# Performance work log

Measured on AMD Instinct MI355X. Metric: run time of the kernel, lower is better.

## Reference

```python
import jax, jax.numpy as jnp
import numpy as np
from jax import lax

GAP_PENALTY = 0.0
TEMPERATURE = 1.0
B, A, L, D, K = 64, 26, 384, 512, 18


def setup_inputs() -> dict:
    key = jax.random.key(0)
    k1, k2, k3, k4 = jax.random.split(key, 4)
    matrices = jax.random.normal(k1, (B, A, L), dtype=jnp.float32)
    # ragged lengths: (len_i, len_0) per pair, in [L//2, L]
    shapes = jax.random.randint(k2, (B, 2), L // 2, L + 1, dtype=jnp.int32)
    s = 1.0 / np.sqrt(A * K)  # torch Conv1d default init scale
    conv_w = jax.random.uniform(k3, (D, A, K), minval=-s, maxval=s, dtype=jnp.float32)
    conv_b = jax.random.uniform(k4, (D,), minval=-s, maxval=s, dtype=jnp.float32)
    return {"matrices": matrices, "shapes": shapes, "conv_w": conv_w, "conv_b": conv_b}


def _smoothmax3(a, b, c, t):
    # t * log(exp(a/t) + exp(b/t) + exp(c/t)), numerically stable
    m = jnp.maximum(jnp.maximum(a, b), c)
    return m + t * jnp.log(jnp.exp((a - m) / t) + jnp.exp((b - m) / t) + jnp.exp((c - m) / t))


def _nw_matrix(sim, t, g):
    # sim: (L, L). Returns smoothed NW value matrix V: (L+1, L+1).
    # V[i,j] = sim[i-1,j-1] + smoothmax(V[i-1,j-1], V[i-1,j]-g, V[i,j-1]-g)
    n = sim.shape[0]
    row0 = -g * jnp.arange(n + 1, dtype=sim.dtype)  # free/affine leading gaps on top row

    def row_step(prev_row, inp):
        s_row, i = inp  # s_row: (L,)
        v_left0 = -g * i  # V[i, 0]

        def col_step(left, xs):
            s, diag, up = xs
            v = s + _smoothmax3(diag, up - g, left - g, t)
            return v, v

        _, rest = lax.scan(col_step, v_left0, (s_row, prev_row[:-1], prev_row[1:]))
        new_row = jnp.concatenate([v_left0[None], rest])
        return new_row, new_row

    _, rows = lax.scan(row_step, row0, (sim, jnp.arange(1, n + 1, dtype=sim.dtype)))
    return jnp.concatenate([row0[None], rows], axis=0)


def needleman_wunsch(sim, shapes, gap_penalty, temperature):
    # sim: (B, L, L) similarity vs sequence 0; shapes: (B, 2) int lengths.
    # Soft alignment posterior = grad of smoothed terminal score wrt similarity.
    li = jnp.clip(shapes[:, 0], 0, sim.shape[1])
    lj = jnp.clip(shapes[:, 1], 0, sim.shape[2])

    def total_score(s):
        V = jax.vmap(lambda m: _nw_matrix(m, temperature, gap_penalty))(s)  # (B, L+1, L+1)
        b = jnp.arange(s.shape[0])
        return jnp.sum(V[b, li, lj])

    return jax.grad(total_score)(sim)  # (B, L, L), expected match matrix


def reference(matrices, shapes, conv_w, conv_b):
    # Conv1d padding='same' with even kernel: torch pads (k-1)//2 left, k//2 right
    k = conv_w.shape[-1]
    pad = ((k - 1) // 2, k // 2)
    emb = lax.conv_general_dilated(
        matrices, conv_w, window_strides=(1,), padding=[pad],
        dimension_numbers=("NCH", "OIH", "NCH"),
    ) + conv_b[None, :, None]  # (B, D, L)
    e = jnp.transpose(emb, (0, 2, 1))  # (B, L, D)
    sim = jnp.einsum("bld,md->blm", e, e[0])  # (B, L_i, L_0): similarity vs sequence 0
    align = needleman_wunsch(sim, shapes, GAP_PENALTY, TEMPERATURE)  # (B, L, L)
    m = jnp.transpose(matrices, (0, 2, 1))  # (B, L, A)
    # consensus in sequence-0 coordinates, then project back to each sequence
    consensus = jnp.mean(jnp.einsum("nia,nij->nja", m, align), axis=0)  # (L, A)
    return jnp.einsum("ja,nij->nia", consensus, align)  # (B, L, A)
```

## Files before the change

### kernel.cpp

```cpp
#include <hip/hip_runtime.h>
#include <hip/hip_bf16.h>
#include <math.h>

#define B_  64
#define A_  26
#define L_  384
#define D_  512
#define K_  18
#define LP1 385
#define VS  384

typedef __attribute__((ext_vector_type(8))) short bf16x8;
typedef __attribute__((ext_vector_type(4))) float f32x4;
typedef unsigned short ushort_t;
typedef unsigned int uint_t;

__device__ __forceinline__ ushort_t f2bf(float v) {
    uint_t u = __float_as_uint(v);
    uint_t r = (u + 0x7FFFu + ((u >> 16) & 1u)) >> 16;
    return (ushort_t)r;
}

__device__ __forceinline__ float dpp_up1(float x) {
    return __int_as_float(__builtin_amdgcn_update_dpp(
        0, __float_as_int(x), 0x138, 0xF, 0xF, true));
}
__device__ __forceinline__ float dpp_down1(float x) {
    return __int_as_float(__builtin_amdgcn_update_dpp(
        0, __float_as_int(x), 0x130, 0xF, 0xF, true));
}

__global__ void transpose_w_kernel(const float* __restrict__ w, float* __restrict__ wt) {
    int o = blockIdx.x * blockDim.x + threadIdx.x;
    int total = A_ * K_ * D_;
    if (o >= total) return;
    int d = o % D_;
    int r = o / D_;
    wt[o] = w[(size_t)d * (A_ * K_) + r];
}

__global__ __launch_bounds__(512) void conv_kernel(const float* __restrict__ x,
                                                   const float* __restrict__ wt,
                                                   const float* __restrict__ bias,
                                                   ushort_t* __restrict__ ehi,
                                                   ushort_t* __restrict__ elo) {
    const int TL = 32;
    const int XW = TL + K_ - 1;
    int l0 = blockIdx.x * TL;
    int b  = blockIdx.y;
    int d  = threadIdx.x;
    __shared__ float xs[A_][XW];
    for (int idx = threadIdx.x; idx < A_ * XW; idx += 512) {
        int a = idx / XW, p = idx % XW;
        int g = l0 - (K_ - 1) / 2 + p;
        xs[a][p] = (g >= 0 && g < L_) ? x[((size_t)b * A_ + a) * L_ + g] : 0.0f;
    }
    __syncthreads();
    float acc[TL];
#pragma unroll
    for (int l = 0; l < TL; ++l) acc[l] = 0.0f;
#pragma unroll 1
    for (int a = 0; a < A_; ++a) {
        float xr[XW];
#pragma unroll
        for (int p = 0; p < XW; ++p) xr[p] = xs[a][p];
        const float* wrow = wt + (size_t)(a * K_) * D_ + d;
#pragma unroll
        for (int k = 0; k < K_; ++k) {
            float w = wrow[(size_t)k * D_];
#pragma unroll
            for (int l = 0; l < TL; ++l)
                acc[l] = fmaf(xr[k + l], w, acc[l]);
        }
    }
    float bv = bias[d];
#pragma unroll
    for (int l = 0; l < TL; ++l) {
        float v = acc[l] + bv;
        ushort_t h = f2bf(v);
        float hf = __uint_as_float(((uint_t)h) << 16);
        ushort_t lo = f2bf(v - hf);
        size_t idx = ((size_t)b * L_ + (l0 + l)) * D_ + d;
        ehi[idx] = h;
        elo[idx] = lo;
    }
}

__global__ __launch_bounds__(256) void sim_kernel(const ushort_t* __restrict__ ehi,
                                                  const ushort_t* __restrict__ elo,
                                                  float* __restrict__ sim) {
    int b = blockIdx.z;
    int w = threadIdx.x >> 6;
    int lane = threadIdx.x & 63;
    int l0 = blockIdx.y * 64 + 32 * (w >> 1);
    int m0 = blockIdx.x * 64 + 32 * (w & 1);
    int r = lane & 15, g = lane >> 4;
    size_t rowA = ((size_t)b * L_ + l0 + r) * D_ + g * 8;
    size_t rowB = ((size_t)m0 + r) * D_ + g * 8;
    const ushort_t* pah = ehi + rowA;
    const ushort_t* pal = elo + rowA;
    const ushort_t* pbh = ehi + rowB;
    const ushort_t* pbl = elo + rowB;
    f32x4 acc00 = {0.f, 0.f, 0.f, 0.f}, acc01 = acc00, acc10 = acc00, acc11 = acc00;
#pragma unroll 2
    for (int ks = 0; ks < 16; ++ks) {
        int off = ks * 32;
        bf16x8 Ah0 = *(const bf16x8*)(pah + off);
        bf16x8 Ah1 = *(const bf16x8*)(pah + 16 * D_ + off);
        bf16x8 Al0 = *(const bf16x8*)(pal + off);
        bf16x8 Al1 = *(const bf16x8*)(pal + 16 * D_ + off);
        bf16x8 Bh0 = *(const bf16x8*)(pbh + off);
        bf16x8 Bh1 = *(const bf16x8*)(pbh + 16 * D_ + off);
        bf16x8 Bl0 = *(const bf16x8*)(pbl + off);
        bf16x8 Bl1 = *(const bf16x8*)(pbl + 16 * D_ + off);
        acc00 = __builtin_amdgcn_mfma_f32_16x16x32_bf16(Ah0, Bh0, acc00, 0, 0, 0);
        acc00 = __builtin_amdgcn_mfma_f32_16x16x32_bf16(Ah0, Bl0, acc00, 0, 0, 0);
        acc00 = __builtin_amdgcn_mfma_f32_16x16x32_bf16(Al0, Bh0, acc00, 0, 0, 0);
        acc01 = __builtin_amdgcn_mfma_f32_16x16x32_bf16(Ah0, Bh1, acc01, 0, 0, 0);
        acc01 = __builtin_amdgcn_mfma_f32_16x16x32_bf16(Ah0, Bl1, acc01, 0, 0, 0);
        acc01 = __builtin_amdgcn_mfma_f32_16x16x32_bf16(Al0, Bh1, acc01, 0, 0, 0);
        acc10 = __builtin_amdgcn_mfma_f32_16x16x32_bf16(Ah1, Bh0, acc10, 0, 0, 0);
        acc10 = __builtin_amdgcn_mfma_f32_16x16x32_bf16(Ah1, Bl0, acc10, 0, 0, 0);
        acc10 = __builtin_amdgcn_mfma_f32_16x16x32_bf16(Al1, Bh0, acc10, 0, 0, 0);
        acc11 = __builtin_amdgcn_mfma_f32_16x16x32_bf16(Ah1, Bh1, acc11, 0, 0, 0);
        acc11 = __builtin_amdgcn_mfma_f32_16x16x32_bf16(Ah1, Bl1, acc11, 0, 0, 0);
        acc11 = __builtin_amdgcn_mfma_f32_16x16x32_bf16(Al1, Bh1, acc11, 0, 0, 0);
    }
    float* sp = sim + ((size_t)b * L_ + l0) * L_ + m0;
#pragma unroll
    for (int v = 0; v < 4; ++v) {
        int row = g * 4 + v;
        sp[(size_t)row * L_ + r]             = acc00[v];
        sp[(size_t)row * L_ + 16 + r]        = acc01[v];
        sp[(size_t)(16 + row) * L_ + r]      = acc10[v];
        sp[(size_t)(16 + row) * L_ + 16 + r] = acc11[v];
    }
}

__global__ __launch_bounds__(64, 1) void nw_fwd_kernel(const float* __restrict__ sim, float* __restrict__ V) {
    int b = blockIdx.x;
    int l = threadIdx.x;
    const float* sb = sim + (size_t)b * L_ * L_;
    float* Vb = V + (size_t)b * L_ * L_;
    const float* srow[6];
    float* vrow[6];
#pragma unroll
    for (int r = 0; r < 6; ++r) {
        srow[r] = sb + (size_t)(6 * l + r) * L_;
        vrow[r] = Vb + (size_t)(6 * l + r) * VS;
    }
    float vleft[6] = {0.f, 0.f, 0.f, 0.f, 0.f, 0.f};
    float bcarry[4] = {0.f, 0.f, 0.f, 0.f};
    float bprev = 0.f;
    float4 snxt[6];
    {
        int c0n = min(max(4 * (0 - l), 0), 380);
#pragma unroll
        for (int r = 0; r < 6; ++r) snxt[r] = *(const float4*)(srow[r] + c0n);
    }
#pragma unroll 1
    for (int T = 0; T < 159; ++T) {
        float sc[6][4];
#pragma unroll
        for (int r = 0; r < 6; ++r) {
            float4 t = snxt[r];
            sc[r][0] = t.x; sc[r][1] = t.y; sc[r][2] = t.z; sc[r][3] = t.w;
        }
        int c0n = min(max(4 * (T + 1 - l), 0), 380);
#pragma unroll
        for (int r = 0; r < 6; ++r) snxt[r] = *(const float4*)(srow[r] + c0n);
        float d0 = dpp_up1(bprev);
        float uin[4];
#pragma unroll
        for (int q = 0; q < 4; ++q) uin[q] = dpp_up1(bcarry[q]);
        int c0 = 4 * (T - l);
        if (c0 >= 0 && c0 <= 380) {
            float vout[6][4];
#pragma unroll
            for (int q = 0; q < 4; ++q) {
                float dg = (q == 0) ? d0 : uin[q - 1];
                float up = uin[q];
#pragma unroll
                for (int r = 0; r < 6; ++r) {
                    float lf = vleft[r];
                    float mx = fmaxf(dg, fmaxf(up, lf));
                    float v = sc[r][q] + mx + __logf(__expf(dg - mx) + __expf(up - mx) + __expf(lf - mx));
                    dg = lf;
                    up = v;
                    vleft[r] = v;
                    vout[r][q] = v;
                }
            }
            bprev = bcarry[3];
#pragma unroll
            for (int q = 0; q < 4; ++q) bcarry[q] = vout[5][q];
#pragma unroll
            for (int r = 0; r < 6; ++r) {
                float4 t;
                t.x = vout[r][0]; t.y = vout[r][1]; t.z = vout[r][2]; t.w = vout[r][3];
                *(float4*)(vrow[r] + c0) = t;
            }
        }
    }
}

__global__ __launch_bounds__(64, 1) void nw_bwd_kernel(const float* __restrict__ sim,
                                                       const float* __restrict__ V,
                                                       const int* __restrict__ shapes,
                                                       float* __restrict__ align_) {
    int b = blockIdx.x;
    int l = threadIdx.x;
    const float* sb = sim + (size_t)b * L_ * L_;
    const float* Vb = V + (size_t)b * L_ * L_;
    float* ab = align_ + (size_t)b * L_ * L_;
    int li = min(max(shapes[2 * b + 0], 0), L_);
    int lj = min(max(shapes[2 * b + 1], 0), L_);
    __shared__ float Eb[2][388];
    for (int k = l; k < 2 * 388; k += 64) ((float*)Eb)[k] = 0.f;
    bool L63 = (l == 63);
#pragma unroll 1
    for (int pass = 0; pass < 3; ++pass) {
        int r0 = 256 - 128 * pass;
        int i1 = r0 + 2 * l + 1, i2 = i1 + 1;
        const float* pV0 = Vb + (size_t)(r0 + 2 * l) * VS;
        const float* pV1 = Vb + (size_t)(r0 + 2 * l + 1) * VS;
        const float* pS0 = sb + (size_t)(r0 + 2 * l) * L_;
        const float* pS1 = sb + (size_t)(r0 + 2 * l + 1) * L_;
        int rb = min(r0 + 128, L_ - 1);
        const float* pV2 = Vb + (size_t)rb * VS;
        const float* pS2 = sb + (size_t)rb * L_;
        float* pE0 = ab + (size_t)(i1 - 1) * L_;
        float* pE1 = ab + (size_t)(i2 - 1) * L_;
        const float* Ebr = Eb[pass & 1];
        float* Ebw = Eb[(pass & 1) ^ 1];
        float e0 = 0.f, e1 = 0.f, u0p = 0.f, u1p = 0.f;
        float ecarry[4] = {0.f, 0.f, 0.f, 0.f};
        float ucarry[4] = {0.f, 0.f, 0.f, 0.f};
        float eprev_s = 0.f, uprev_s = 0.f;
        float eb_carry = 0.f, ub_carry = 0.f;
        float4 nV0, nV1, nS0, nS1, nV2, nS2;
        {
            int c0n = min(max(380 - 4 * (0 - (63 - l)), 0), 380);
            nV0 = *(const float4*)(pV0 + c0n); nV1 = *(const float4*)(pV1 + c0n);
            nS0 = *(const float4*)(pS0 + c0n); nS1 = *(const float4*)(pS1 + c0n);
            nV2 = *(const float4*)(pV2 + c0n); nS2 = *(const float4*)(pS2 + c0n);
        }
#pragma unroll 1
        for (int T = 0; T < 159; ++T) {
            float V0q[4], V1q[4], S0q[4], S1q[4], V2q[4], S2q[4];
            { float4 t = nV0; V0q[0]=t.x; V0q[1]=t.y; V0q[2]=t.z; V0q[3]=t.w; }
            { float4 t = nV1; V1q[0]=t.x; V1q[1]=t.y; V1q[2]=t.z; V1q[3]=t.w; }
            { float4 t = nS0; S0q[0]=t.x; S0q[1]=t.y; S0q[2]=t.z; S0q[3]=t.w; }
            { float4 t = nS1; S1q[0]=t.x; S1q[1]=t.y; S1q[2]=t.z; S1q[3]=t.w; }
            { float4 t = nV2; V2q[0]=t.x; V2q[1]=t.y; V2q[2]=t.z; V2q[3]=t.w; }
            { float4 t = nS2; S2q[0]=t.x; S2q[1]=t.y; S2q[2]=t.z; S2q[3]=t.w; }
            int m = T - (63 - l);
            int c0 = 380 - 4 * m;
            int c0n = min(max(c0 - 4, 0), 380);
            nV0 = *(const float4*)(pV0 + c0n); nV1 = *(const float4*)(pV1 + c0n);
            nS0 = *(const float4*)(pS0 + c0n); nS1 = *(const float4*)(pS1 + c0n);
            nV2 = *(const float4*)(pV2 + c0n); nS2 = *(const float4*)(pS2 + c0n);
            float enbtd3 = dpp_down1(eprev_s);
            float unbtd3 = dpp_down1(uprev_s);
            float enbc[4], unbc[4];
#pragma unroll
            for (int q = 0; q < 4; ++q) {
                enbc[q] = dpp_down1(ecarry[q]);
                unbc[q] = dpp_down1(ucarry[q]);
            }
            eprev_s = e0; uprev_s = u0p;
            if (c0 >= 0 && c0 <= 380) {
                float ebq[4] = {0.f, 0.f, 0.f, 0.f};
                if (L63) {
                    float4 t = *(const float4*)&Ebr[c0];
                    ebq[0] = t.x; ebq[1] = t.y; ebq[2] = t.z; ebq[3] = t.w;
                }
                float u63q[4], u0c[4], u1c[4];
#pragma unroll
                for (int q = 0; q < 4; ++q) {
                    u63q[q] = V2q[q] - S2q[q];
                    u0c[q]  = V0q[q] - S0q[q];
                    u1c[q]  = V1q[q] - S1q[q];
                }
                float Eo0[4], Eo1[4];
#pragma unroll
                for (int qq = 0; qq < 4; ++qq) {
                    const int q = 3 - qq;
                    int j = c0 + 1 + q;
                    float enb   = L63 ? ebq[q]  : enbc[q];
                    float unb   = L63 ? u63q[q] : unbc[q];
                    float enbtd = (q == 3) ? (L63 ? eb_carry : enbtd3)
                                           : (L63 ? ebq[q + 1] : enbc[q + 1]);
                    float unbtd = (q == 3) ? (L63 ? ub_carry : unbtd3)
                                           : (L63 ? u63q[q + 1] : unbc[q + 1]);
                    bool jlt = (j < L_), i2lt = (i2 < L_);
                    float wtd1 = (i2lt && jlt) ? __expf(V1q[q] - unbtd) : 0.f;
                    float wtu1 = i2lt ? __expf(V1q[q] - unb) : 0.f;
                    float wtl1 = jlt ? __expf(V1q[q] - u1p) : 0.f;
                    float wtd0 = jlt ? __expf(V0q[q] - u1p) : 0.f;
                    float wtu0 = __expf(V0q[q] - u1c[q]);
                    float wtl0 = jlt ? __expf(V0q[q] - u0p) : 0.f;
                    float ea1 = (i2 == li && j == lj) ? 1.f : 0.f;
                    ea1 += wtd1 * enbtd + wtu1 * enb + wtl1 * e1;
                    float ea0 = (i1 == li && j == lj) ? 1.f : 0.f;
                    ea0 += wtd0 * e1 + wtu0 * ea1 + wtl0 * e0;
                    e1 = ea1; e0 = ea0;
                    u1p = u1c[q]; u0p = u0c[q];
                    Eo1[q] = ea1; Eo0[q] = ea0;
                }
                eb_carry = ebq[0]; ub_carry = u63q[0];
#pragma unroll
                for (int q = 0; q < 4; ++q) { ecarry[q] = Eo0[q]; ucarry[q] = u0c[q]; }
                float4 t0, t1;
                t0.x = Eo0[0]; t0.y = Eo0[1]; t0.z = Eo0[2]; t0.w = Eo0[3];
                t1.x = Eo1[0]; t1.y = Eo1[1]; t1.z = Eo1[2]; t1.w = Eo1[3];
                *(float4*)(pE0 + c0) = t0;
                *(float4*)(pE1 + c0) = t1;
                if (l == 0) *(float4*)&Ebw[c0] = t0;
            }
        }
    }
}

__global__ __launch_bounds__(256) void consensus_kernel(const float* __restrict__ x,
                                                        const float* __restrict__ align_,
                                                        float* __restrict__ cons) {
    int n  = blockIdx.y;
    int j0 = blockIdx.x * 64;
    __shared__ float ms[A_][L_];
    for (int idx = threadIdx.x; idx < A_ * L_; idx += 256)
        ((float*)ms)[idx] = x[(size_t)n * A_ * L_ + idx];
    __syncthreads();
    int jl = threadIdx.x & 63;
    int g  = threadIdx.x >> 6;
    int a0 = g * 7;
    int na = (a0 + 7 <= A_) ? 7 : (A_ - a0);
    int j  = j0 + jl;
    float acc[7] = {0.f, 0.f, 0.f, 0.f, 0.f, 0.f, 0.f};
    const float* acol = align_ + (size_t)n * L_ * L_ + j;
    for (int i = 0; i < L_; ++i) {
        float al = acol[(size_t)i * L_];
#pragma unroll
        for (int t = 0; t < 7; ++t)
            if (t < na) acc[t] = fmaf(al, ms[a0 + t][i], acc[t]);
    }
    for (int t = 0; t < na; ++t)
        atomicAdd(&cons[(size_t)j * A_ + a0 + t], acc[t] * (1.0f / B_));
}

__global__ __launch_bounds__(256) void out_kernel(const float* __restrict__ align_,
                                                  const float* __restrict__ cons,
                                                  float* __restrict__ out) {
    int n  = blockIdx.y;
    int i0 = blockIdx.x * 32;
    __shared__ float cs[L_][A_];
    __shared__ float as_[32][L_ + 1];
    for (int idx = threadIdx.x; idx < L_ * A_; idx += 256)
        ((float*)cs)[idx] = cons[idx];
    for (int idx = threadIdx.x; idx < 32 * L_; idx += 256) {
        int r = idx / L_, c = idx % L_;
        as_[r][c] = align_[((size_t)n * L_ + i0 + r) * L_ + c];
    }
    __syncthreads();
    for (int o = threadIdx.x; o < 32 * A_; o += 256) {
        int il = o / A_, a = o % A_;
        float s = 0.f;
        for (int jj = 0; jj < L_; ++jj)
            s = fmaf(as_[il][jj], cs[jj][a], s);
        out[((size_t)n * L_ + i0 + il) * A_ + a] = s;
    }
}

extern "C" void kernel_launch(void* const* d_in, const int* in_sizes, int n_in,
                              void* d_out, int out_size, void* d_ws, size_t ws_size,
                              hipStream_t stream) {
    const float* matrices = (const float*)d_in[0];
    const int*   shapes   = (const int*)d_in[1];
    const float* conv_w   = (const float*)d_in[2];
    const float* conv_b   = (const float*)d_in[3];
    float* out = (float*)d_out;

    char* p = (char*)d_ws;
    ushort_t* ehi = (ushort_t*)p;  p += (size_t)B_ * L_ * D_ * 2;
    ushort_t* elo = (ushort_t*)p;  p += (size_t)B_ * L_ * D_ * 2;
    float* sim    = (float*)p;     p += (size_t)B_ * L_ * L_ * 4;
    float* V      = (float*)p;     p += (size_t)B_ * L_ * L_ * 4;
    float* align_ = (float*)p;     p += (size_t)B_ * L_ * L_ * 4;
    float* wt     = (float*)p;     p += (size_t)A_ * K_ * D_ * 4;
    float* cons   = (float*)p;

    transpose_w_kernel<<<(A_ * K_ * D_ + 255) / 256, 256, 0, stream>>>(conv_w, wt);
    conv_kernel<<<dim3(L_ / 32, B_), 512, 0, stream>>>(matrices, wt, conv_b, ehi, elo);
    sim_kernel<<<dim3(L_ / 64, L_ / 64, B_), 256, 0, stream>>>(ehi, elo, sim);
    nw_fwd_kernel<<<B_, 64, 0, stream>>>(sim, V);
    nw_bwd_kernel<<<B_, 64, 0, stream>>>(sim, V, shapes, align_);
    hipMemsetAsync(cons, 0, (size_t)L_ * A_ * sizeof(float), stream);
    consensus_kernel<<<dim3(L_ / 64, B_), 256, 0, stream>>>(matrices, align_, cons);
    out_kernel<<<dim3(L_ / 32, B_), 256, 0, stream>>>(align_, cons, out);
}
```

Before: 1.089 ms.

## Store sim, V and alignment in anti-diagonal wavefront layout for NW kernels

Stores the similarity, value and alignment matrices in a diagonal-major layout, so each wavefront step of the NW forward and backward scans reads and writes one contiguous 1536-float block across the 64 lanes. The backward kernel is rewritten to match the forward decomposition: one pass of 6 rows per lane with DPP neighbour exchange, replacing three 128-row passes that handed boundaries through shared memory. Loads are prefetched several diagonals ahead with rotating register buffers. The consensus and output kernels index the new layout, and the alignment buffer reuses the embedding workspace. The cost is scattered stores in sim_kernel and strided gathers in the consumer kernels.

Result: faster. 990.8 us (-9.0%).

```diff
diff --git a/kernel.cpp b/kernel.cpp
--- a/kernel.cpp
+++ b/kernel.cpp
@@ -7,13 +7,17 @@
 #define L_  384
 #define D_  512
 #define K_  18
-#define LP1 385
-#define VS  384
+#define SZD 245760
 
 typedef __attribute__((ext_vector_type(8))) short bf16x8;
 typedef __attribute__((ext_vector_type(4))) float f32x4;
 typedef unsigned short ushort_t;
 typedef unsigned int uint_t;
+
+__device__ __forceinline__ void stD(float* sp, int z, int c, float v) {
+    int dl = z / 6, dr = z - dl * 6;
+    sp[(size_t)(dl + (c >> 2)) * 1536 + dr * 256 + dl * 4 + (c & 3)] = v;
+}
 
 __device__ __forceinline__ ushort_t f2bf(float v) {
     uint_t u = __float_as_uint(v);
@@ -88,7 +92,7 @@
 
 __global__ __launch_bounds__(256) void sim_kernel(const ushort_t* __restrict__ ehi,
                                                   const ushort_t* __restrict__ elo,
-                                                  float* __restrict__ sim) {
+                                                  float* __restrict__ simD) {
     int b = blockIdx.z;
     int w = threadIdx.x >> 6;
     int lane = threadIdx.x & 63;
@@ -126,54 +130,42 @@
         acc11 = __builtin_amdgcn_mfma_f32_16x16x32_bf16(Ah1, Bl1, acc11, 0, 0, 0);
         acc11 = __builtin_amdgcn_mfma_f32_16x16x32_bf16(Al1, Bh1, acc11, 0, 0, 0);
     }
-    float* sp = sim + ((size_t)b * L_ + l0) * L_ + m0;
+    float* sp = simD + (size_t)b * SZD;
 #pragma unroll
     for (int v = 0; v < 4; ++v) {
-        int row = g * 4 + v;
-        sp[(size_t)row * L_ + r]             = acc00[v];
-        sp[(size_t)row * L_ + 16 + r]        = acc01[v];
-        sp[(size_t)(16 + row) * L_ + r]      = acc10[v];
-        sp[(size_t)(16 + row) * L_ + 16 + r] = acc11[v];
-    }
-}
-
-__global__ __launch_bounds__(64, 1) void nw_fwd_kernel(const float* __restrict__ sim, float* __restrict__ V) {
+        int ar0 = l0 + g * 4 + v, ar1 = ar0 + 16;
+        int ac0 = m0 + r,         ac1 = ac0 + 16;
+        stD(sp, ar0, ac0, acc00[v]);
+        stD(sp, ar0, ac1, acc01[v]);
+        stD(sp, ar1, ac0, acc10[v]);
+        stD(sp, ar1, ac1, acc11[v]);
+    }
+}
+
+__global__ __launch_bounds__(64, 1) void nw_fwd_kernel(const float* __restrict__ simD, float* __restrict__ VD) {
     int b = blockIdx.x;
     int l = threadIdx.x;
-    const float* sb = sim + (size_t)b * L_ * L_;
-    float* Vb = V + (size_t)b * L_ * L_;
-    const float* srow[6];
-    float* vrow[6];
-#pragma unroll
-    for (int r = 0; r < 6; ++r) {
-        srow[r] = sb + (size_t)(6 * l + r) * L_;
-        vrow[r] = Vb + (size_t)(6 * l + r) * VS;
-    }
+    const float* pS = simD + (size_t)b * SZD + l * 4;
+    float*       pV = VD   + (size_t)b * SZD + l * 4;
     float vleft[6] = {0.f, 0.f, 0.f, 0.f, 0.f, 0.f};
     float bcarry[4] = {0.f, 0.f, 0.f, 0.f};
     float bprev = 0.f;
-    float4 snxt[6];
-    {
-        int c0n = min(max(4 * (0 - l), 0), 380);
-#pragma unroll
-        for (int r = 0; r < 6; ++r) snxt[r] = *(const float4*)(srow[r] + c0n);
-    }
-#pragma unroll 1
-    for (int T = 0; T < 159; ++T) {
+
+    auto body = [&](float4* buf, int Tb) {
         float sc[6][4];
 #pragma unroll
         for (int r = 0; r < 6; ++r) {
-            float4 t = snxt[r];
+            float4 t = buf[r];
             sc[r][0] = t.x; sc[r][1] = t.y; sc[r][2] = t.z; sc[r][3] = t.w;
         }
-        int c0n = min(max(4 * (T + 1 - l), 0), 380);
-#pragma unroll
-        for (int r = 0; r < 6; ++r) snxt[r] = *(const float4*)(srow[r] + c0n);
+        int dP = min(Tb + 3, 158);
+#pragma unroll
+        for (int r = 0; r < 6; ++r) buf[r] = *(const float4*)(pS + dP * 1536 + r * 256);
         float d0 = dpp_up1(bprev);
         float uin[4];
 #pragma unroll
         for (int q = 0; q < 4; ++q) uin[q] = dpp_up1(bcarry[q]);
-        int c0 = 4 * (T - l);
+        int c0 = 4 * (Tb - l);
         if (c0 >= 0 && c0 <= 380) {
             float vout[6][4];
 #pragma unroll
@@ -198,132 +190,135 @@
             for (int r = 0; r < 6; ++r) {
                 float4 t;
                 t.x = vout[r][0]; t.y = vout[r][1]; t.z = vout[r][2]; t.w = vout[r][3];
-                *(float4*)(vrow[r] + c0) = t;
+                *(float4*)(pV + Tb * 1536 + r * 256) = t;
             }
         }
-    }
-}
-
-__global__ __launch_bounds__(64, 1) void nw_bwd_kernel(const float* __restrict__ sim,
-                                                       const float* __restrict__ V,
+    };
+
+    float4 buf0[6], buf1[6], buf2[6];
+#pragma unroll
+    for (int r = 0; r < 6; ++r) {
+        buf0[r] = *(const float4*)(pS + 0 * 1536 + r * 256);
+        buf1[r] = *(const float4*)(pS + 1 * 1536 + r * 256);
+        buf2[r] = *(const float4*)(pS + 2 * 1536 + r * 256);
+    }
+#pragma unroll 1
+    for (int Tb = 0; Tb < 159; Tb += 3) {
+        body(buf0, Tb);
+        body(buf1, Tb + 1);
+        body(buf2, Tb + 2);
+    }
+}
+
+__global__ __launch_bounds__(64, 1) void nw_bwd_kernel(const float* __restrict__ simD,
+                                                       const float* __restrict__ VD,
                                                        const int* __restrict__ shapes,
-                                                       float* __restrict__ align_) {
+                                                       float* __restrict__ ED) {
     int b = blockIdx.x;
     int l = threadIdx.x;
-    const float* sb = sim + (size_t)b * L_ * L_;
-    const float* Vb = V + (size_t)b * L_ * L_;
-    float* ab = align_ + (size_t)b * L_ * L_;
+    const float* pS = simD + (size_t)b * SZD + l * 4;
+    const float* pV = VD   + (size_t)b * SZD + l * 4;
+    float*       pE = ED   + (size_t)b * SZD + l * 4;
     int li = min(max(shapes[2 * b + 0], 0), L_);
     int lj = min(max(shapes[2 * b + 1], 0), L_);
-    __shared__ float Eb[2][388];
-    for (int k = l; k < 2 * 388; k += 64) ((float*)Eb)[k] = 0.f;
-    bool L63 = (l == 63);
+    float e[6] = {0.f, 0.f, 0.f, 0.f, 0.f, 0.f};
+    float u[6] = {0.f, 0.f, 0.f, 0.f, 0.f, 0.f};
+    float ecar[4] = {0.f, 0.f, 0.f, 0.f};
+    float ucar[4] = {0.f, 0.f, 0.f, 0.f};
+    float eprev_s = 0.f, uprev_s = 0.f;
+
+    auto body = [&](float4* bufV, float4* bufS, int T) {
+        float Vq[6][4], Sq[6][4];
+#pragma unroll
+        for (int r = 0; r < 6; ++r) {
+            float4 tv = bufV[r], ts = bufS[r];
+            Vq[r][0] = tv.x; Vq[r][1] = tv.y; Vq[r][2] = tv.z; Vq[r][3] = tv.w;
+            Sq[r][0] = ts.x; Sq[r][1] = ts.y; Sq[r][2] = ts.z; Sq[r][3] = ts.w;
+        }
+        int dP = max(158 - T - 2, 0);
+#pragma unroll
+        for (int r = 0; r < 6; ++r) {
+            bufV[r] = *(const float4*)(pV + dP * 1536 + r * 256);
+            bufS[r] = *(const float4*)(pS + dP * 1536 + r * 256);
+        }
+        float enbtd_s = dpp_down1(eprev_s);
+        float unbtd_s = dpp_down1(uprev_s);
+        float enb_c[4], unb_c[4];
+#pragma unroll
+        for (int q = 0; q < 4; ++q) {
+            enb_c[q] = dpp_down1(ecar[q]);
+            unb_c[q] = dpp_down1(ucar[q]);
+        }
+        eprev_s = e[0]; uprev_s = u[0];
+        int ct = 158 - T - l;
+        if (ct >= 0 && ct <= 95) {
+            float Eo[6][4];
+#pragma unroll
+            for (int qq = 0; qq < 4; ++qq) {
+                const int q = 3 - qq;
+                int j = 4 * ct + q + 1;
+                bool jlt = (j < L_);
+                float eo[6], uo[6];
+#pragma unroll
+                for (int r = 0; r < 6; ++r) { eo[r] = e[r]; uo[r] = u[r]; }
+#pragma unroll
+                for (int rr = 0; rr < 6; ++rr) {
+                    const int r = 5 - rr;
+                    int i = 6 * l + r + 1;
+                    bool ilt = (i < L_);
+                    float Vv = Vq[r][q];
+                    float u_new = Vv - Sq[r][q];
+                    float eb_old, ub_old, eb_new, ub_new;
+                    if (r == 5) {
+                        eb_old = (q == 3) ? enbtd_s : enb_c[q + 1];
+                        ub_old = (q == 3) ? unbtd_s : unb_c[q + 1];
+                        eb_new = enb_c[q];
+                        ub_new = unb_c[q];
+                    } else {
+                        eb_old = eo[r + 1]; ub_old = uo[r + 1];
+                        eb_new = e[r + 1];  ub_new = u[r + 1];
+                    }
+                    float wtd = (ilt && jlt) ? __expf(Vv - ub_old) : 0.f;
+                    float wtu = ilt ? __expf(Vv - ub_new) : 0.f;
+                    float wtl = jlt ? __expf(Vv - uo[r]) : 0.f;
+                    float en = (i == li && j == lj) ? 1.f : 0.f;
+                    en += wtd * eb_old + wtu * eb_new + wtl * eo[r];
+                    e[r] = en; u[r] = u_new;
+                    Eo[r][q] = en;
+                }
+            }
+#pragma unroll
+            for (int q = 0; q < 4; ++q) {
+                ecar[q] = Eo[0][q];
+                ucar[q] = Vq[0][q] - Sq[0][q];
+            }
+            float* pEd = pE + (size_t)(158 - T) * 1536;
+#pragma unroll
+            for (int r = 0; r < 6; ++r) {
+                float4 t;
+                t.x = Eo[r][0]; t.y = Eo[r][1]; t.z = Eo[r][2]; t.w = Eo[r][3];
+                *(float4*)(pEd + r * 256) = t;
+            }
+        }
+    };
+
+    float4 bufVA[6], bufSA[6], bufVB[6], bufSB[6];
+#pragma unroll
+    for (int r = 0; r < 6; ++r) {
+        bufVA[r] = *(const float4*)(pV + 158 * 1536 + r * 256);
+        bufSA[r] = *(const float4*)(pS + 158 * 1536 + r * 256);
+        bufVB[r] = *(const float4*)(pV + 157 * 1536 + r * 256);
+        bufSB[r] = *(const float4*)(pS + 157 * 1536 + r * 256);
+    }
 #pragma unroll 1
-    for (int pass = 0; pass < 3; ++pass) {
-        int r0 = 256 - 128 * pass;
-        int i1 = r0 + 2 * l + 1, i2 = i1 + 1;
-        const float* pV0 = Vb + (size_t)(r0 + 2 * l) * VS;
-        const float* pV1 = Vb + (size_t)(r0 + 2 * l + 1) * VS;
-        const float* pS0 = sb + (size_t)(r0 + 2 * l) * L_;
-        const float* pS1 = sb + (size_t)(r0 + 2 * l + 1) * L_;
-        int rb = min(r0 + 128, L_ - 1);
-        const float* pV2 = Vb + (size_t)rb * VS;
-        const float* pS2 = sb + (size_t)rb * L_;
-        float* pE0 = ab + (size_t)(i1 - 1) * L_;
-        float* pE1 = ab + (size_t)(i2 - 1) * L_;
-        const float* Ebr = Eb[pass & 1];
-        float* Ebw = Eb[(pass & 1) ^ 1];
-        float e0 = 0.f, e1 = 0.f, u0p = 0.f, u1p = 0.f;
-        float ecarry[4] = {0.f, 0.f, 0.f, 0.f};
-        float ucarry[4] = {0.f, 0.f, 0.f, 0.f};
-        float eprev_s = 0.f, uprev_s = 0.f;
-        float eb_carry = 0.f, ub_carry = 0.f;
-        float4 nV0, nV1, nS0, nS1, nV2, nS2;
-        {
-            int c0n = min(max(380 - 4 * (0 - (63 - l)), 0), 380);
-            nV0 = *(const float4*)(pV0 + c0n); nV1 = *(const float4*)(pV1 + c0n);
-            nS0 = *(const float4*)(pS0 + c0n); nS1 = *(const float4*)(pS1 + c0n);
-            nV2 = *(const float4*)(pV2 + c0n); nS2 = *(const float4*)(pS2 + c0n);
-        }
-#pragma unroll 1
-        for (int T = 0; T < 159; ++T) {
-            float V0q[4], V1q[4], S0q[4], S1q[4], V2q[4], S2q[4];
-            { float4 t = nV0; V0q[0]=t.x; V0q[1]=t.y; V0q[2]=t.z; V0q[3]=t.w; }
-            { float4 t = nV1; V1q[0]=t.x; V1q[1]=t.y; V1q[2]=t.z; V1q[3]=t.w; }
-            { float4 t = nS0; S0q[0]=t.x; S0q[1]=t.y; S0q[2]=t.z; S0q[3]=t.w; }
-            { float4 t = nS1; S1q[0]=t.x; S1q[1]=t.y; S1q[2]=t.z; S1q[3]=t.w; }
-            { float4 t = nV2; V2q[0]=t.x; V2q[1]=t.y; V2q[2]=t.z; V2q[3]=t.w; }
-            { float4 t = nS2; S2q[0]=t.x; S2q[1]=t.y; S2q[2]=t.z; S2q[3]=t.w; }
-            int m = T - (63 - l);
-            int c0 = 380 - 4 * m;
-            int c0n = min(max(c0 - 4, 0), 380);
-            nV0 = *(const float4*)(pV0 + c0n); nV1 = *(const float4*)(pV1 + c0n);
-            nS0 = *(const float4*)(pS0 + c0n); nS1 = *(const float4*)(pS1 + c0n);
-            nV2 = *(const float4*)(pV2 + c0n); nS2 = *(const float4*)(pS2 + c0n);
-            float enbtd3 = dpp_down1(eprev_s);
-            float unbtd3 = dpp_down1(uprev_s);
-            float enbc[4], unbc[4];
-#pragma unroll
-            for (int q = 0; q < 4; ++q) {
-                enbc[q] = dpp_down1(ecarry[q]);
-                unbc[q] = dpp_down1(ucarry[q]);
-            }
-            eprev_s = e0; uprev_s = u0p;
-            if (c0 >= 0 && c0 <= 380) {
-                float ebq[4] = {0.f, 0.f, 0.f, 0.f};
-                if (L63) {
-                    float4 t = *(const float4*)&Ebr[c0];
-                    ebq[0] = t.x; ebq[1] = t.y; ebq[2] = t.z; ebq[3] = t.w;
-                }
-                float u63q[4], u0c[4], u1c[4];
-#pragma unroll
-                for (int q = 0; q < 4; ++q) {
-                    u63q[q] = V2q[q] - S2q[q];
-                    u0c[q]  = V0q[q] - S0q[q];
-                    u1c[q]  = V1q[q] - S1q[q];
-                }
-                float Eo0[4], Eo1[4];
-#pragma unroll
-                for (int qq = 0; qq < 4; ++qq) {
-                    const int q = 3 - qq;
-                    int j = c0 + 1 + q;
-                    float enb   = L63 ? ebq[q]  : enbc[q];
-                    float unb   = L63 ? u63q[q] : unbc[q];
-                    float enbtd = (q == 3) ? (L63 ? eb_carry : enbtd3)
-                                           : (L63 ? ebq[q + 1] : enbc[q + 1]);
-                    float unbtd = (q == 3) ? (L63 ? ub_carry : unbtd3)
-                                           : (L63 ? u63q[q + 1] : unbc[q + 1]);
-                    bool jlt = (j < L_), i2lt = (i2 < L_);
-                    float wtd1 = (i2lt && jlt) ? __expf(V1q[q] - unbtd) : 0.f;
-                    float wtu1 = i2lt ? __expf(V1q[q] - unb) : 0.f;
-                    float wtl1 = jlt ? __expf(V1q[q] - u1p) : 0.f;
-                    float wtd0 = jlt ? __expf(V0q[q] - u1p) : 0.f;
-                    float wtu0 = __expf(V0q[q] - u1c[q]);
-                    float wtl0 = jlt ? __expf(V0q[q] - u0p) : 0.f;
-                    float ea1 = (i2 == li && j == lj) ? 1.f : 0.f;
-                    ea1 += wtd1 * enbtd + wtu1 * enb + wtl1 * e1;
-                    float ea0 = (i1 == li && j == lj) ? 1.f : 0.f;
-                    ea0 += wtd0 * e1 + wtu0 * ea1 + wtl0 * e0;
-                    e1 = ea1; e0 = ea0;
-                    u1p = u1c[q]; u0p = u0c[q];
-                    Eo1[q] = ea1; Eo0[q] = ea0;
-                }
-                eb_carry = ebq[0]; ub_carry = u63q[0];
-#pragma unroll
-                for (int q = 0; q < 4; ++q) { ecarry[q] = Eo0[q]; ucarry[q] = u0c[q]; }
-                float4 t0, t1;
-                t0.x = Eo0[0]; t0.y = Eo0[1]; t0.z = Eo0[2]; t0.w = Eo0[3];
-                t1.x = Eo1[0]; t1.y = Eo1[1]; t1.z = Eo1[2]; t1.w = Eo1[3];
-                *(float4*)(pE0 + c0) = t0;
-                *(float4*)(pE1 + c0) = t1;
-                if (l == 0) *(float4*)&Ebw[c0] = t0;
-            }
-        }
+    for (int T = 0; T < 160; T += 2) {
+        body(bufVA, bufSA, T);
+        body(bufVB, bufSB, T + 1);
     }
 }
 
 __global__ __launch_bounds__(256) void consensus_kernel(const float* __restrict__ x,
-                                                        const float* __restrict__ align_,
+                                                        const float* __restrict__ ED,
                                                         float* __restrict__ cons) {
     int n  = blockIdx.y;
     int j0 = blockIdx.x * 64;
@@ -337,18 +332,24 @@
     int na = (a0 + 7 <= A_) ? 7 : (A_ - a0);
     int j  = j0 + jl;
     float acc[7] = {0.f, 0.f, 0.f, 0.f, 0.f, 0.f, 0.f};
-    const float* acol = align_ + (size_t)n * L_ * L_ + j;
-    for (int i = 0; i < L_; ++i) {
-        float al = acol[(size_t)i * L_];
-#pragma unroll
-        for (int t = 0; t < 7; ++t)
-            if (t < na) acc[t] = fmaf(al, ms[a0 + t][i], acc[t]);
+    const float* aB = ED + (size_t)n * SZD + (j >> 2) * 1536 + (j & 3);
+#pragma unroll 1
+    for (int dl = 0; dl < 64; ++dl) {
+        const float* ap = aB + dl * 1540;
+#pragma unroll
+        for (int dr = 0; dr < 6; ++dr) {
+            float al = ap[dr * 256];
+            int i = dl * 6 + dr;
+#pragma unroll
+            for (int t = 0; t < 7; ++t)
+                if (t < na) acc[t] = fmaf(al, ms[a0 + t][i], acc[t]);
+        }
     }
     for (int t = 0; t < na; ++t)
         atomicAdd(&cons[(size_t)j * A_ + a0 + t], acc[t] * (1.0f / B_));
 }
 
-__global__ __launch_bounds__(256) void out_kernel(const float* __restrict__ align_,
+__global__ __launch_bounds__(256) void out_kernel(const float* __restrict__ ED,
                                                   const float* __restrict__ cons,
                                                   float* __restrict__ out) {
     int n  = blockIdx.y;
@@ -357,9 +358,12 @@
     __shared__ float as_[32][L_ + 1];
     for (int idx = threadIdx.x; idx < L_ * A_; idx += 256)
         ((float*)cs)[idx] = cons[idx];
+    const float* aB = ED + (size_t)n * SZD;
     for (int idx = threadIdx.x; idx < 32 * L_; idx += 256) {
-        int r = idx / L_, c = idx % L_;
-        as_[r][c] = align_[((size_t)n * L_ + i0 + r) * L_ + c];
+        int r = idx / L_, c = idx - r * L_;
+        int z = i0 + r;
+        int dl = z / 6, dr = z - dl * 6;
+        as_[r][c] = aB[(size_t)(dl + (c >> 2)) * 1536 + dr * 256 + dl * 4 + (c & 3)];
     }
     __syncthreads();
     for (int o = threadIdx.x; o < 32 * A_; o += 256) {
@@ -381,20 +385,20 @@
     float* out = (float*)d_out;
 
     char* p = (char*)d_ws;
-    ushort_t* ehi = (ushort_t*)p;  p += (size_t)B_ * L_ * D_ * 2;
-    ushort_t* elo = (ushort_t*)p;  p += (size_t)B_ * L_ * D_ * 2;
-    float* sim    = (float*)p;     p += (size_t)B_ * L_ * L_ * 4;
-    float* V      = (float*)p;     p += (size_t)B_ * L_ * L_ * 4;
-    float* align_ = (float*)p;     p += (size_t)B_ * L_ * L_ * 4;
-    float* wt     = (float*)p;     p += (size_t)A_ * K_ * D_ * 4;
-    float* cons   = (float*)p;
+    float*    ED  = (float*)p;
+    ushort_t* ehi = (ushort_t*)p;
+    ushort_t* elo = ehi + (size_t)B_ * L_ * D_;
+    float* simD = (float*)(p + (size_t)B_ * SZD * 4);
+    float* VD   = simD + (size_t)B_ * SZD;
+    float* wt   = VD + (size_t)B_ * SZD;
+    float* cons = wt + (size_t)A_ * K_ * D_;
 
     transpose_w_kernel<<<(A_ * K_ * D_ + 255) / 256, 256, 0, stream>>>(conv_w, wt);
     conv_kernel<<<dim3(L_ / 32, B_), 512, 0, stream>>>(matrices, wt, conv_b, ehi, elo);
-    sim_kernel<<<dim3(L_ / 64, L_ / 64, B_), 256, 0, stream>>>(ehi, elo, sim);
-    nw_fwd_kernel<<<B_, 64, 0, stream>>>(sim, V);
-    nw_bwd_kernel<<<B_, 64, 0, stream>>>(sim, V, shapes, align_);
+    sim_kernel<<<dim3(L_ / 64, L_ / 64, B_), 256, 0, stream>>>(ehi, elo, simD);
+    nw_fwd_kernel<<<B_, 64, 0, stream>>>(simD, VD);
+    nw_bwd_kernel<<<B_, 64, 0, stream>>>(simD, VD, shapes, ED);
     hipMemsetAsync(cons, 0, (size_t)L_ * A_ * sizeof(float), stream);
-    consensus_kernel<<<dim3(L_ / 64, B_), 256, 0, stream>>>(matrices, align_, cons);
-    out_kernel<<<dim3(L_ / 32, B_), 256, 0, stream>>>(align_, cons, out);
-}
+    consensus_kernel<<<dim3(L_ / 64, B_), 256, 0, stream>>>(matrices, ED, cons);
+    out_kernel<<<dim3(L_ / 32, B_), 256, 0, stream>>>(ED, cons, out);
+}
```
